# Optimization experiments

Hardware: AMD Instinct MI355X
Metric: run time of the kernel (lower is better)

## Reference

```python
import jax, jax.numpy as jnp
import numpy as np

ALPHA, BETA, INIT_P = 100.0, 1000.0, 2.0
K_NEIGHBORS = 24


def index_points(pts, idx):
    # pts: [B,N,C], idx: [B,...] int -> [B,...,C]
    B = pts.shape[0]
    b = jnp.arange(B).reshape((B,) + (1,) * (idx.ndim - 1))
    return pts[b, idx]


def fps(xyz, m):
    # furthest point sampling, deterministic start at index 0. xyz: [B,N,3]
    B, N, _ = xyz.shape
    def step(carry, _):
        dist, far = carry
        centroid = xyz[jnp.arange(B), far]              # [B,3]
        d = jnp.sum((xyz - centroid[:, None, :]) ** 2, -1)
        dist = jnp.minimum(dist, d)
        nxt = jnp.argmax(dist, -1).astype(jnp.int32)
        return (dist, nxt), far
    init = (jnp.full((B, N), 1e10, xyz.dtype), jnp.zeros((B,), jnp.int32))
    _, idx = jax.lax.scan(step, init, None, length=m)
    return idx.T                                        # [B,m]


def knn_indices(k, xyz, centers):
    # squared distances [B,G,N], k smallest
    d = (jnp.sum(centers ** 2, -1)[..., None]
         - 2.0 * jnp.einsum('bgc,bnc->bgn', centers, xyz)
         + jnp.sum(xyz ** 2, -1)[:, None, :])
    _, idx = jax.lax.top_k(-d, k)
    return idx                                          # [B,G,K]


def normalize(x, ref):
    # torch: mean = ref.unsqueeze(-2); std over ALL elements of (x-mean), ddof=1
    d = x - ref[..., None, :]
    std = jnp.std(d, ddof=1)
    return d / (std + 1e-5)


def fourier_map(t, Bmat):
    # t: [B,7,G,K]; Bmat: [7, C//2] (already includes scale) -> [B,C,G,K]
    x = jnp.transpose(t, (0, 2, 3, 1))                  # [B,G,K,7]
    proj = 2.0 * jnp.pi * (x @ Bmat)                    # [B,G,K,C/2]
    f = jnp.concatenate([jnp.sin(proj), jnp.cos(proj)], -1)
    f = jnp.sign(f) * jnp.abs(f) ** 5
    return jnp.transpose(f, (0, 3, 1, 2))


def tr_embed(my_dim, t):
    # t: [B,3,G,K] -> [B,my_dim,G,K]
    B, C, G, K = t.shape
    F = my_dim // (2 * C)
    dim_embed = ALPHA ** (jnp.arange(F, dtype=t.dtype) / F)
    div = BETA * t[..., None] / dim_embed               # [B,3,G,K,F]
    pe = jnp.stack([jnp.sin(div), jnp.cos(div)], -1).reshape(B, C, G, K, 2 * F)
    pe = jnp.transpose(pe, (0, 1, 4, 2, 3)).reshape(B, my_dim, G, K)
    return pe


def lga(lc_xyz, lc_x, knn_xyz, knn_x, Bmat):
    B, G, K, C = knn_x.shape
    knn_x = normalize(knn_x, lc_x)
    knn_xyz = normalize(knn_xyz, lc_xyz)
    lc_rep = jnp.transpose(jnp.broadcast_to(lc_xyz[:, :, None, :], (B, G, K, 3)), (0, 3, 1, 2))
    knn_xyz_t = jnp.transpose(knn_xyz, (0, 3, 1, 2))    # [B,3,G,K]
    knn_x_t = jnp.transpose(knn_x, (0, 3, 1, 2))        # [B,C,G,K]
    cross = jnp.cross(knn_xyz_t, lc_rep, axis=1)
    dot = jnp.sum(knn_xyz_t * lc_rep, 1, keepdims=True)
    emb_in = jnp.concatenate([knn_xyz_t, cross, dot], 1)  # [B,7,G,K]
    emb = fourier_map(emb_in, Bmat)                       # [B,C,G,K]
    knn_x_w = jnp.concatenate([knn_x_t, emb], 1)          # [B,2C,G,K]
    pe = tr_embed(2 * C, knn_xyz_t) + tr_embed(2 * C, lc_rep)
    return (knn_x_w + pe) * pe


def k_anp(x):
    # x: [B,2C,G,K], data-dependent p-norm attention over K
    std = jnp.std(x, axis=-1, ddof=1, keepdims=True)
    p = jax.lax.stop_gradient(INIT_P + jnp.log1p(std.mean()))  # torch uses .item()
    norm = jnp.sum(jnp.abs(x) ** p, -1, keepdims=True) ** (1.0 / p)
    lc = norm / (norm + 1e-8)
    e = jnp.exp(lc)
    return (x * e).mean(-1) / e.mean(-1)                # [B,2C,G]


def bn_gelu(x, gamma, beta):
    # BatchNorm1d in training mode (batch stats, biased var) + exact GELU
    mean = x.mean((0, 2), keepdims=True)
    var = ((x - mean) ** 2).mean((0, 2), keepdims=True)
    y = (x - mean) / jnp.sqrt(var + 1e-5) * gamma[None, :, None] + beta[None, :, None]
    return jax.nn.gelu(y, approximate=False)


def stage(xyz, x, group_num, Bmat, gamma, beta):
    # xyz: [B,N,3]; x: [B,C,N]
    feats = jnp.transpose(x, (0, 2, 1))
    fi = fps(xyz, group_num)
    lc_xyz = index_points(xyz, fi)
    lc_x = index_points(feats, fi)
    ki = knn_indices(K_NEIGHBORS, xyz, lc_xyz)
    knn_xyz = index_points(xyz, ki)
    knn_x = index_points(feats, ki)
    w = lga(lc_xyz, lc_x, knn_xyz, knn_x, Bmat)
    pooled = k_anp(w) + w.mean(-1)                      # [B,2C,G]
    return lc_xyz, bn_gelu(pooled, gamma, beta)


def setup_inputs() -> dict:
    key = jax.random.key(0)
    k1, k2, k3, k4 = jax.random.split(key, 4)
    B, N, C0 = 4, 4096, 72
    return {
        'xyz': jax.random.uniform(k1, (B, N, 3), jnp.float32),
        'x': jax.random.normal(k2, (B, C0, N), jnp.float32),
        'fourier_B0': jax.random.normal(k3, (7, C0 // 2), jnp.float32) * 50.0,
        'fourier_B1': jax.random.normal(k4, (7, C0), jnp.float32) * 50.0,
        'bn_gamma0': jnp.ones((2 * C0,), jnp.float32),
        'bn_beta0': jnp.zeros((2 * C0,), jnp.float32),
        'bn_gamma1': jnp.ones((4 * C0,), jnp.float32),
        'bn_beta1': jnp.zeros((4 * C0,), jnp.float32),
    }


def reference(xyz, x, fourier_B0, fourier_B1, bn_gamma0, bn_beta0, bn_gamma1, bn_beta1):
    N = xyz.shape[1]
    xyz, x = stage(xyz, x, N // 2, fourier_B0, bn_gamma0, bn_beta0)   # -> [B,144,2048]
    xyz, x = stage(xyz, x, N // 4, fourier_B1, bn_gamma1, bn_beta1)   # -> [B,288,1024]
    return x
```

## Files before the change

kernel.cpp:

```cpp
#include <hip/hip_runtime.h>
#include <math.h>

#define KNB 24

typedef float v2f __attribute__((ext_vector_type(2)));

__global__ void k_transpose(const float* __restrict__ x, float* __restrict__ feats,
                            int B, int C, int N) {
    int idx = blockIdx.x * blockDim.x + threadIdx.x;
    int tot = B * C * N;
    if (idx >= tot) return;
    int n = idx % N; int t = idx / N; int c = t % C; int b = t / C;
    feats[((size_t)b * N + n) * C + c] = x[idx];
}

template<int CTRL>
__device__ __forceinline__ float dppmax(float v) {
    int t = __builtin_amdgcn_update_dpp(0, __float_as_int(v), CTRL, 0xf, 0xf, true);
    return fmaxf(v, __int_as_float(t));
}
template<int CTRL>
__device__ __forceinline__ unsigned dppmaxu(unsigned v) {
    unsigned t = (unsigned)__builtin_amdgcn_update_dpp(0, (int)v, CTRL, 0xf, 0xf, true);
    return v > t ? v : t;
}

template<int NPT, int NWAVE>
__global__ __launch_bounds__(64 * NWAVE) void k_fps_t(const float* __restrict__ xyz,
                                                      int* __restrict__ fi,
                                                      int N, int M) {
#pragma clang fp contract(off)
    const int NP2 = NPT / 2;
    const int b = blockIdx.x;
    const int tid = threadIdx.x;
    const int lane = tid & 63;
    const int wid = tid >> 6;
    extern __shared__ char smc[];
    unsigned long long* keys = (unsigned long long*)smc;
    int* fi_lds = (int*)(smc + 2 * NWAVE * 8);
    size_t poff = ((size_t)(2 * NWAVE * 8) + (size_t)M * 4 + 15) & ~(size_t)15;
    float4* pts = (float4*)(smc + poff);

    const float* p = xyz + (size_t)b * N * 3;
    for (int i = tid; i < N; i += 64 * NWAVE)
        pts[i] = make_float4(p[i*3], p[i*3+1], p[i*3+2], 0.0f);
    __syncthreads();

    const int base = tid * NPT;
    v2f rx[NP2], ry[NP2], rz[NP2], dist[NP2];
#pragma unroll
    for (int j = 0; j < NP2; ++j) {
        float4 a = pts[base + 2*j];
        float4 c = pts[base + 2*j + 1];
        rx[j] = (v2f){a.x, c.x}; ry[j] = (v2f){a.y, c.y}; rz[j] = (v2f){a.z, c.z};
        dist[j] = (v2f){1e10f, 1e10f};
    }

    int far = 0;
    float4 cpt = pts[0];
    float cx = cpt.x, cy = cpt.y, cz = cpt.z;
    for (int it = 0; it < M; ++it) {
        if (tid == 0) fi_lds[it] = far;
        v2f cx2 = (v2f){cx, cx}, cy2 = (v2f){cy, cy}, cz2 = (v2f){cz, cz};
        v2f bv2 = (v2f){-1.0f, -1.0f};
#pragma unroll
        for (int j = 0; j < NP2; ++j) {
            v2f dx = rx[j] - cx2, dy = ry[j] - cy2, dz = rz[j] - cz2;
            v2f d = (dx*dx + dy*dy) + dz*dz;
            v2f dd = __builtin_elementwise_min(dist[j], d);
            dist[j] = dd;
            bv2 = __builtin_elementwise_max(bv2, dd);
        }
        float bv = fmaxf(bv2.x, bv2.y);
        int bi = 0;
#pragma unroll
        for (int j = NP2 - 1; j >= 0; --j) {
            if (dist[j].y == bv) bi = base + 2*j + 1;
            if (dist[j].x == bv) bi = base + 2*j;
        }
        float r = bv;
        r = dppmax<0x111>(r); r = dppmax<0x112>(r);
        r = dppmax<0x114>(r); r = dppmax<0x118>(r);
        r = dppmax<0x142>(r); r = dppmax<0x143>(r);
        float wmax = __int_as_float(__builtin_amdgcn_readlane(__float_as_int(r), 63));
        unsigned long long mask = __ballot(bv == wmax);
        int src = __builtin_ctzll(mask);
        int wbi = __builtin_amdgcn_readlane(bi, src);
        unsigned long long key =
            ((unsigned long long)__float_as_uint(wmax) << 32) | (unsigned)(~wbi);
        if (lane == 0) keys[(it & 1) * NWAVE + wid] = key;
        __syncthreads();
        unsigned long long k0 = keys[(it & 1) * NWAVE + 0];
#pragma unroll
        for (int w = 1; w < NWAVE; ++w) {
            unsigned long long kw = keys[(it & 1) * NWAVE + w];
            if (kw > k0) k0 = kw;
        }
        far = (int)(~(unsigned)k0);
        float4 c = pts[far];
        cx = c.x; cy = c.y; cz = c.z;
    }
    __syncthreads();
    for (int i = tid; i < M; i += 64 * NWAVE) fi[b * M + i] = fi_lds[i];
}

template<int NPT>
__global__ __launch_bounds__(256) void k_knn_t(const float* __restrict__ xyz,
                                               const float* __restrict__ feats,
                                               const int* __restrict__ fi,
                                               float* __restrict__ lc_xyz,
                                               float* __restrict__ lc_x,
                                               int* __restrict__ ki,
                                               double* __restrict__ part,
                                               int B, int N, int G, int C, int identity) {
#pragma clang fp contract(off)
    int bg = blockIdx.x; int b = bg / G; int g = bg % G;
    int idx = identity ? g : fi[bg];
    const int tid = threadIdx.x;
    const int lane = tid & 63;
    const int wid = tid >> 6;
    __shared__ unsigned long long keys[2][4];
    __shared__ int kis[KNB];
    __shared__ float cfeat[144];
    const float* p = xyz + (size_t)b * N * 3;
    float cx = p[idx*3], cy = p[idx*3+1], cz = p[idx*3+2];
    if (tid < 3) lc_xyz[(size_t)bg * 3 + tid] = p[idx*3 + tid];
    for (int c = tid; c < C; c += 256) {
        float v = feats[((size_t)b * N + idx) * C + c];
        lc_x[(size_t)bg * C + c] = v;
        cfeat[c] = v;
    }
    float cc = (cx*cx + cy*cy) + cz*cz;
    const int base = tid * NPT;
    float dist[NPT];
#pragma unroll
    for (int j = 0; j < NPT; ++j) {
        float x0 = p[(base+j)*3], x1 = p[(base+j)*3+1], x2 = p[(base+j)*3+2];
        float xx = (x0*x0 + x1*x1) + x2*x2;
        float dt = (cx*x0 + cy*x1) + cz*x2;
        dist[j] = (cc - 2.0f*dt) + xx;
    }
    for (int kk = 0; kk < KNB; ++kk) {
        float bv = 1e30f;
#pragma unroll
        for (int j = 0; j < NPT; ++j) bv = fminf(bv, dist[j]);
        int lj = 0;
#pragma unroll
        for (int j = NPT - 1; j >= 0; --j) if (dist[j] == bv) lj = j;
        unsigned ub = ~__float_as_uint(bv);
        unsigned r = ub;
        r = dppmaxu<0x111>(r); r = dppmaxu<0x112>(r);
        r = dppmaxu<0x114>(r); r = dppmaxu<0x118>(r);
        r = dppmaxu<0x142>(r); r = dppmaxu<0x143>(r);
        unsigned uwin = (unsigned)__builtin_amdgcn_readlane((int)r, 63);
        unsigned long long mask = __ballot(ub == uwin);
        int src = __builtin_ctzll(mask);
        int gi = __builtin_amdgcn_readlane(base + lj, src);
        unsigned long long key = ((unsigned long long)uwin << 32) | (unsigned)(~gi);
        if (lane == 0) keys[kk & 1][wid] = key;
        __syncthreads();
        unsigned long long k0 = keys[kk & 1][0];
#pragma unroll
        for (int w = 1; w < 4; ++w) {
            unsigned long long kw = keys[kk & 1][w];
            if (kw > k0) k0 = kw;
        }
        int win = (int)(~(unsigned)k0);
        if (tid == 0) kis[kk] = win;
        if (win >= base && win < base + NPT) {
            int wj = win - base;
#pragma unroll
            for (int j = 0; j < NPT; ++j) if (j == wj) dist[j] = 1e30f;
        }
    }
    __syncthreads();
    if (tid < KNB) ki[(size_t)bg * KNB + tid] = kis[tid];
    double s = 0.0, s2 = 0.0, s3 = 0.0, s4 = 0.0;
    for (int i = tid; i < KNB * C; i += 256) {
        int k = i / C, c = i - k * C;
        float d = feats[((size_t)b * N + kis[k]) * C + c] - cfeat[c];
        s += (double)d; s2 += (double)d * (double)d;
    }
    if (tid < KNB * 3) {
        int k = tid / 3, c = tid - k * 3;
        float ctr = (c == 0) ? cx : ((c == 1) ? cy : cz);
        float d = p[kis[k] * 3 + c] - ctr;
        s3 += (double)d; s4 += (double)d * (double)d;
    }
    for (int off = 32; off > 0; off >>= 1) {
        s += __shfl_down(s, off); s2 += __shfl_down(s2, off);
        s3 += __shfl_down(s3, off); s4 += __shfl_down(s4, off);
    }
    __shared__ double sw[4][4];
    if ((tid & 63) == 0) {
        sw[wid][0] = s; sw[wid][1] = s2; sw[wid][2] = s3; sw[wid][3] = s4;
    }
    __syncthreads();
    if (tid == 0) {
        double t0 = 0.0, t1 = 0.0, t2 = 0.0, t3 = 0.0;
        for (int w = 0; w < 4; ++w) {
            t0 += sw[w][0]; t1 += sw[w][1]; t2 += sw[w][2]; t3 += sw[w][3];
        }
        double* q = part + (size_t)bg * 4;
        q[0] = t0; q[1] = t1; q[2] = t2; q[3] = t3;
    }
}

__global__ __launch_bounds__(1024) void k_reduce(const double* __restrict__ part,
                                                 double* __restrict__ acc, int n) {
    double s0 = 0.0, s1 = 0.0, s2 = 0.0, s3 = 0.0;
    for (int i = threadIdx.x; i < n; i += 1024) {
        const double* q = part + (size_t)i * 4;
        s0 += q[0]; s1 += q[1]; s2 += q[2]; s3 += q[3];
    }
    for (int off = 32; off > 0; off >>= 1) {
        s0 += __shfl_down(s0, off); s1 += __shfl_down(s1, off);
        s2 += __shfl_down(s2, off); s3 += __shfl_down(s3, off);
    }
    __shared__ double sw[16][4];
    int wid = threadIdx.x >> 6;
    if ((threadIdx.x & 63) == 0) {
        sw[wid][0] = s0; sw[wid][1] = s1; sw[wid][2] = s2; sw[wid][3] = s3;
    }
    __syncthreads();
    if (threadIdx.x == 0) {
        double t0 = 0.0, t1 = 0.0, t2 = 0.0, t3 = 0.0;
        for (int w = 0; w < 16; ++w) {
            t0 += sw[w][0]; t1 += sw[w][1]; t2 += sw[w][2]; t3 += sw[w][3];
        }
        acc[0] = t0; acc[1] = t1; acc[2] = t2; acc[3] = t3;
    }
}

__global__ __launch_bounds__(256) void k_feature(
    const float* __restrict__ xyz, const float* __restrict__ feats,
    const float* __restrict__ lc_xyz, const float* __restrict__ lc_x,
    const int* __restrict__ ki, const float* __restrict__ Bmat,
    const double* __restrict__ accp, float* __restrict__ pooled,
    int B, int N, int G, int C, double nx, double nz)
{
    int bg = blockIdx.x; int b = bg / G; int g = bg % G;
    int tid = threadIdx.x;
    int C2 = C >> 1;
    int Cout = 2 * C;
    int F = C / 3;
    extern __shared__ float sm[];
    float* t7    = sm;
    float* sxyzn = t7 + KNB * 7;
    int*   kidx  = (int*)(sxyzn + KNB * 3);
    float* semb  = (float*)(kidx + KNB);

    double a0 = accp[0], a1 = accp[1], a2 = accp[2], a3 = accp[3];
    double vx = (a1 - a0 * a0 / nx) / (nx - 1.0);
    float invx = 1.0f / (sqrtf((float)vx) + 1e-5f);
    double vz = (a3 - a2 * a2 / nz) / (nz - 1.0);
    float invz = 1.0f / (sqrtf((float)vz) + 1e-5f);

    float l0 = lc_xyz[(size_t)bg*3], l1 = lc_xyz[(size_t)bg*3+1], l2 = lc_xyz[(size_t)bg*3+2];

    if (tid < KNB) {
        int idx = ki[(size_t)bg * KNB + tid];
        kidx[tid] = idx;
        const float* q = xyz + ((size_t)b * N + idx) * 3;
        float a0f = (q[0]-l0)*invz, a1f = (q[1]-l1)*invz, a2f = (q[2]-l2)*invz;
        float c0 = a1f*l2 - a2f*l1;
        float c1 = a2f*l0 - a0f*l2;
        float c2 = a0f*l1 - a1f*l0;
        float dt = (a0f*l0 + a1f*l1) + a2f*l2;
        float* tp = t7 + tid * 7;
        tp[0]=a0f; tp[1]=a1f; tp[2]=a2f; tp[3]=c0; tp[4]=c1; tp[5]=c2; tp[6]=dt;
        sxyzn[tid*3]=a0f; sxyzn[tid*3+1]=a1f; sxyzn[tid*3+2]=a2f;
    }
    __syncthreads();
    const float TWO_PI = 6.2831854820251465f;
    for (int i = tid; i < KNB * C2; i += blockDim.x) {
        int k = i / C2, m2 = i % C2;
        const float* tp = t7 + k * 7;
        float s = 0.0f;
        for (int j = 0; j < 7; ++j) s += tp[j] * Bmat[j * C2 + m2];
        float pr = TWO_PI * s;
        float sn, cs;
        __sincosf(pr, &sn, &cs);
        float sn2 = sn*sn, cs2 = cs*cs;
        semb[k*C + m2]      = sn2*sn2*sn;
        semb[k*C + C2 + m2] = cs2*cs2*cs;
    }
    __syncthreads();
    for (int m = tid; m < Cout; m += blockDim.x) {
        int c3 = m / (2 * F);
        int r  = m % (2 * F);
        int f  = r >> 1;
        int trig = r & 1;
        float de = __powf(100.0f, (float)f / (float)F);
        float rde = 1000.0f / de;
        float lv = (c3 == 0) ? l0 : ((c3 == 1) ? l1 : l2);
        float a2v = lv * rde;
        float pe2 = trig ? __cosf(a2v) : __sinf(a2v);
        float lfm = (m < C) ? lc_x[(size_t)bg * C + m] : 0.0f;
        float acc = 0.0f;
        for (int k = 0; k < KNB; ++k) {
            float v;
            if (m < C) {
                v = (feats[((size_t)b * N + kidx[k]) * C + m] - lfm) * invx;
            } else {
                v = semb[k * C + (m - C)];
            }
            float a1v = sxyzn[k*3 + c3] * rde;
            float pe1 = trig ? __cosf(a1v) : __sinf(a1v);
            float pe = pe1 + pe2;
            acc += (v + pe) * pe;
        }
        float mean = acc / 24.0f;
        pooled[((size_t)b * Cout + m) * G + g] = 2.0f * mean;
    }
}

__global__ __launch_bounds__(256) void k_bn(const float* __restrict__ pooled,
                                            const float* __restrict__ gamma,
                                            const float* __restrict__ beta,
                                            float* __restrict__ out,
                                            int B, int Cout, int G, int transposed) {
    int m = blockIdx.x;
    double s = 0.0, s2 = 0.0;
    for (int i = threadIdx.x; i < B * G; i += 256) {
        int b = i / G, g = i % G;
        float v = pooled[((size_t)b * Cout + m) * G + g];
        s += (double)v; s2 += (double)v * (double)v;
    }
    for (int off = 32; off > 0; off >>= 1) { s += __shfl_down(s, off); s2 += __shfl_down(s2, off); }
    __shared__ double sw[4], sw2[4];
    __shared__ float smv[2];
    int wid = threadIdx.x >> 6;
    if ((threadIdx.x & 63) == 0) { sw[wid] = s; sw2[wid] = s2; }
    __syncthreads();
    if (threadIdx.x == 0) {
        double ts = sw[0] + sw[1] + sw[2] + sw[3];
        double ts2 = sw2[0] + sw2[1] + sw2[2] + sw2[3];
        double n = (double)(B * G);
        double mean = ts / n;
        double var = ts2 / n - mean * mean;
        smv[0] = (float)mean; smv[1] = (float)var;
    }
    __syncthreads();
    float mean = smv[0], var = smv[1];
    float ga = gamma[m], be = beta[m];
    for (int i = threadIdx.x; i < B * G; i += 256) {
        int b = i / G, g = i % G;
        float v = pooled[((size_t)b * Cout + m) * G + g];
        float y = (v - mean) / sqrtf(var + 1e-5f) * ga + be;
        float ge = 0.5f * y * (1.0f + erff(y / 1.4142135381698608f));
        if (transposed) out[((size_t)b * G + g) * Cout + m] = ge;
        else            out[((size_t)b * Cout + m) * G + g] = ge;
    }
}

extern "C" void kernel_launch(void* const* d_in, const int* in_sizes, int n_in,
                              void* d_out, int out_size, void* d_ws, size_t ws_size,
                              hipStream_t stream) {
    const int B = 4, N1 = 4096, C0 = 72, G1 = 2048, Co1 = 144;
    const int N2 = 2048, C1 = 144, G2 = 1024, Co2 = 288;

    const float* xyz = (const float*)d_in[0];
    const float* x0  = (const float*)d_in[1];
    const float* B0  = (const float*)d_in[2];
    const float* B1  = (const float*)d_in[3];
    const float* g0  = (const float*)d_in[4];
    const float* be0 = (const float*)d_in[5];
    const float* g1  = (const float*)d_in[6];
    const float* be1 = (const float*)d_in[7];
    float* out = (float*)d_out;

    char* wp = (char*)d_ws;
    size_t off = 0;
    auto A = [&](size_t bytes) -> void* {
        void* p = wp + off;
        off += (bytes + 255) & ~(size_t)255;
        return p;
    };
    float* feats1  = (float*)A((size_t)B*N1*C0*4);
    int*   fi1     = (int*)  A((size_t)B*G1*4);
    float* lcx1    = (float*)A((size_t)B*G1*3*4);
    float* lcf1    = (float*)A((size_t)B*G1*C0*4);
    int*   ki1     = (int*)  A((size_t)B*G1*KNB*4);
    double* acc    = (double*)A(8*8);
    double* part   = (double*)A((size_t)B*G1*4*8);
    float* pooled1 = (float*)A((size_t)B*Co1*G1*4);
    float* feats2  = (float*)A((size_t)B*N2*C1*4);
    float* lcx2    = (float*)A((size_t)B*G2*3*4);
    float* lcf2    = lcf1;
    int*   ki2     = ki1;
    float* pooled2 = feats1;

    k_transpose<<<(B*C0*N1 + 255)/256, 256, 0, stream>>>(x0, feats1, B, C0, N1);

    {
        size_t poff = ((size_t)(2*4*8) + (size_t)G1*4 + 15) & ~(size_t)15;
        size_t shm = poff + (size_t)N1*16;
        k_fps_t<16, 4><<<B, 256, shm, stream>>>(xyz, fi1, N1, G1);
    }
    k_knn_t<16><<<B*G1, 256, 0, stream>>>(xyz, feats1, fi1, lcx1, lcf1, ki1, part,
                                          B, N1, G1, C0, 0);
    k_reduce<<<1, 1024, 0, stream>>>(part, acc, B*G1);
    {
        size_t shf = (size_t)(KNB*7 + KNB*3 + KNB + KNB*C0) * 4;
        k_feature<<<B*G1, 256, shf, stream>>>(xyz, feats1, lcx1, lcf1, ki1, B0, acc, pooled1,
                                              B, N1, G1, C0,
                                              (double)B*G1*KNB*C0, (double)B*G1*KNB*3);
    }
    k_bn<<<Co1, 256, 0, stream>>>(pooled1, g0, be0, feats2, B, Co1, G1, 1);

    k_knn_t<8><<<B*G2, 256, 0, stream>>>(lcx1, feats2, (const int*)nullptr,
                                         lcx2, lcf2, ki2, part, B, N2, G2, C1, 1);
    k_reduce<<<1, 1024, 0, stream>>>(part, acc + 4, B*G2);
    {
        size_t shf = (size_t)(KNB*7 + KNB*3 + KNB + KNB*C1) * 4;
        k_feature<<<B*G2, 256, shf, stream>>>(lcx1, feats2, lcx2, lcf2, ki2, B1, acc + 4, pooled2,
                                              B, N2, G2, C1,
                                              (double)B*G2*KNB*C1, (double)B*G2*KNB*3);
    }
    k_bn<<<Co2, 256, 0, stream>>>(pooled2, g1, be1, out, B, Co2, G2, 0);
}
```

Measured before the change: 1.671 ms.

## Run furthest point sampling in a single wave per batch to drop block barriers

```diff
diff --git a/kernel.cpp b/kernel.cpp
--- a/kernel.cpp
+++ b/kernel.cpp
@@ -25,28 +25,21 @@
     return v > t ? v : t;
 }
 
-template<int NPT, int NWAVE>
-__global__ __launch_bounds__(64 * NWAVE) void k_fps_t(const float* __restrict__ xyz,
-                                                      int* __restrict__ fi,
-                                                      int N, int M) {
+template<int NPT>
+__global__ __launch_bounds__(64, 1) void k_fps1(const float* __restrict__ xyz,
+                                                int* __restrict__ fi,
+                                                int N, int M) {
 #pragma clang fp contract(off)
     const int NP2 = NPT / 2;
     const int b = blockIdx.x;
-    const int tid = threadIdx.x;
-    const int lane = tid & 63;
-    const int wid = tid >> 6;
-    extern __shared__ char smc[];
-    unsigned long long* keys = (unsigned long long*)smc;
-    int* fi_lds = (int*)(smc + 2 * NWAVE * 8);
-    size_t poff = ((size_t)(2 * NWAVE * 8) + (size_t)M * 4 + 15) & ~(size_t)15;
-    float4* pts = (float4*)(smc + poff);
-
+    const int lane = threadIdx.x;
+    extern __shared__ float4 pts[];
     const float* p = xyz + (size_t)b * N * 3;
-    for (int i = tid; i < N; i += 64 * NWAVE)
+    for (int i = lane; i < N; i += 64)
         pts[i] = make_float4(p[i*3], p[i*3+1], p[i*3+2], 0.0f);
     __syncthreads();
 
-    const int base = tid * NPT;
+    const int base = lane * NPT;
     v2f rx[NP2], ry[NP2], rz[NP2], dist[NP2];
 #pragma unroll
     for (int j = 0; j < NP2; ++j) {
@@ -60,7 +53,7 @@
     float4 cpt = pts[0];
     float cx = cpt.x, cy = cpt.y, cz = cpt.z;
     for (int it = 0; it < M; ++it) {
-        if (tid == 0) fi_lds[it] = far;
+        if (lane == 0) fi[b * M + it] = far;
         v2f cx2 = (v2f){cx, cx}, cy2 = (v2f){cy, cy}, cz2 = (v2f){cz, cz};
         v2f bv2 = (v2f){-1.0f, -1.0f};
 #pragma unroll
@@ -85,23 +78,10 @@
         float wmax = __int_as_float(__builtin_amdgcn_readlane(__float_as_int(r), 63));
         unsigned long long mask = __ballot(bv == wmax);
         int src = __builtin_ctzll(mask);
-        int wbi = __builtin_amdgcn_readlane(bi, src);
-        unsigned long long key =
-            ((unsigned long long)__float_as_uint(wmax) << 32) | (unsigned)(~wbi);
-        if (lane == 0) keys[(it & 1) * NWAVE + wid] = key;
-        __syncthreads();
-        unsigned long long k0 = keys[(it & 1) * NWAVE + 0];
-#pragma unroll
-        for (int w = 1; w < NWAVE; ++w) {
-            unsigned long long kw = keys[(it & 1) * NWAVE + w];
-            if (kw > k0) k0 = kw;
-        }
-        far = (int)(~(unsigned)k0);
+        far = __builtin_amdgcn_readlane(bi, src);
         float4 c = pts[far];
         cx = c.x; cy = c.y; cz = c.z;
     }
-    __syncthreads();
-    for (int i = tid; i < M; i += 64 * NWAVE) fi[b * M + i] = fi_lds[i];
 }
 
 template<int NPT>
@@ -393,11 +373,7 @@
 
     k_transpose<<<(B*C0*N1 + 255)/256, 256, 0, stream>>>(x0, feats1, B, C0, N1);
 
-    {
-        size_t poff = ((size_t)(2*4*8) + (size_t)G1*4 + 15) & ~(size_t)15;
-        size_t shm = poff + (size_t)N1*16;
-        k_fps_t<16, 4><<<B, 256, shm, stream>>>(xyz, fi1, N1, G1);
-    }
+    k_fps1<64><<<B, 64, (size_t)N1*16, stream>>>(xyz, fi1, N1, G1);
     k_knn_t<16><<<B*G1, 256, 0, stream>>>(xyz, feats1, fi1, lcx1, lcf1, ki1, part,
                                           B, N1, G1, C0, 0);
     k_reduce<<<1, 1024, 0, stream>>>(part, acc, B*G1);
```

Measured after the change: 3.449 ms. +106.3%, slower.
